# Optimization experiments

Hardware: AMD Instinct MI355X
Metric: run time of the kernel (lower is better)

The kernel has to match this reference:

```python
import jax, jax.numpy as jnp
import numpy as np

B, S, H, E, V, T, OOV = 32, 400, 256, 300, 50000, 20, 50


def setup_inputs() -> dict:
    key = jax.random.key(0)
    ks = jax.random.split(key, 24)
    g = lambda k, sh, scale=0.02: jax.random.normal(k, sh, dtype=jnp.float32) * scale
    return {
        "enc_hidden": jax.random.normal(ks[0], (B, S, 2 * H), dtype=jnp.float32),
        "h0": jax.random.normal(ks[1], (B, H), dtype=jnp.float32),
        "c0": jax.random.normal(ks[2], (B, H), dtype=jnp.float32),
        "embedding": g(ks[3], (V, E), 1.0),
        "W_enc": g(ks[4], (2 * H, H)),
        "W_dec": g(ks[5], (H, H)),
        "w_cov": g(ks[6], (H,)),
        "v_attn": g(ks[7], (H,)),
        "W_ih": g(ks[8], (E, 4 * H)),
        "W_hh": g(ks[9], (H, 4 * H)),
        "b_lstm": jnp.zeros((4 * H,), jnp.float32),
        "W_out1": g(ks[10], (3 * H, H)),
        "b_out1": jnp.zeros((H,), jnp.float32),
        "W_out2": g(ks[11], (H, V)),
        "b_out2": jnp.zeros((V,), jnp.float32),
        "w_h": g(ks[12], (2 * H, 1)),
        "w_s": g(ks[13], (H, 1)),
        "w_x": g(ks[14], (E, 1)),
        "b_x": jnp.zeros((1,), jnp.float32),
        "dec_input": jax.random.randint(ks[15], (B, T), 0, V),
        "enc_input_ext": jax.random.randint(ks[16], (B, S), 0, V + OOV),
        "enc_pad_mask": jnp.ones((B, S), dtype=bool),
        "max_oov_len": OOV,
    }


def reference(enc_hidden, h0, c0, embedding, W_enc, W_dec, w_cov, v_attn,
              W_ih, W_hh, b_lstm, W_out1, b_out1, W_out2, b_out2,
              w_h, w_s, w_x, b_x, dec_input, enc_input_ext, enc_pad_mask,
              max_oov_len):
    b, s, two_h = enc_hidden.shape
    enc_feat = enc_hidden @ W_enc  # [B,S,H], precomputed attention keys
    batch_idx = jnp.arange(b)[:, None]
    NEG = jnp.float32(-1e9)

    def step(carry, x_t):
        h, c, cov = carry
        emb = embedding[x_t]  # [B,E]
        # LSTM cell
        gates = emb @ W_ih + h @ W_hh + b_lstm
        i, f, gg, o = jnp.split(gates, 4, axis=-1)
        c = jax.nn.sigmoid(f) * c + jax.nn.sigmoid(i) * jnp.tanh(gg)
        h = jax.nn.sigmoid(o) * jnp.tanh(c)
        # coverage attention over encoder states
        e = jnp.tanh(enc_feat + (h @ W_dec)[:, None, :] + cov[..., None] * w_cov) @ v_attn  # [B,S]
        e = jnp.where(enc_pad_mask, e, NEG)
        attn = jax.nn.softmax(e, axis=-1)
        context = jnp.einsum('bs,bsd->bd', attn, enc_hidden)  # [B,2H]
        cov = cov + attn
        # vocab distribution
        out = jnp.concatenate([h, context], axis=-1) @ W_out1 + b_out1
        vocab_dist = jax.nn.softmax(out @ W_out2 + b_out2, axis=-1)  # [B,V]
        # pointer-generator gate
        p_gen = jax.nn.sigmoid(context @ w_h + h @ w_s + emb @ w_x + b_x)  # [B,1]
        vocab_dist = p_gen * vocab_dist
        weighted_attn = (1.0 - p_gen) * attn
        # extend vocab and scatter-add copy probabilities
        ext = jnp.concatenate(
            [vocab_dist, jnp.zeros((b, max_oov_len), vocab_dist.dtype)], axis=-1)
        final = ext.at[batch_idx, enc_input_ext].add(weighted_attn)
        return (h, c, cov), (final, attn, cov)

    cov0 = jnp.zeros((b, s), jnp.float32)
    _, (finals, attns, covs) = jax.lax.scan(step, (h0, c0, cov0), dec_input.T)
    # stack with time on the last axis, as in the torch module
    return (jnp.moveaxis(finals, 0, -1),
            jnp.moveaxis(attns, 0, -1),
            jnp.moveaxis(covs, 0, -1))
```

## Files before the change

kernel.cpp:

```cpp
#include <hip/hip_runtime.h>
#include <hip/hip_bf16.h>

#define B_    32
#define S_    400
#define H_    256
#define E_    300
#define V_    50000
#define T_    20
#define VE_   50050
#define TB_   640
#define VPAD_ 50048
#define FIN_  32032000
#define NB_   16
#define SC_   25
#define K5NT  8

typedef __attribute__((ext_vector_type(8))) short bf16x8;
typedef __attribute__((ext_vector_type(4))) float f32x4;

__device__ __forceinline__ float sigmoid_f(float x){ return 1.f/(1.f+__expf(-x)); }
__device__ __forceinline__ float tanh_f(float x){ return 1.f - 2.f/(__expf(2.f*x)+1.f); }

__device__ __forceinline__ float bf2f(unsigned short u){
  union { unsigned int i; float f; } x; x.i = ((unsigned int)u) << 16; return x.f;
}
__device__ __forceinline__ unsigned short f2bf(float f){
  union { __hip_bfloat16 h; unsigned short u; } x; x.h = __float2bfloat16(f); return x.u;
}

__device__ __forceinline__ void st_dev(float* p, float v){
  __hip_atomic_store(p, v, __ATOMIC_RELAXED, __HIP_MEMORY_SCOPE_AGENT);
}
__device__ __forceinline__ float ld_dev(const float* p){
  return __hip_atomic_load(p, __ATOMIC_RELAXED, __HIP_MEMORY_SCOPE_AGENT);
}
__device__ __forceinline__ int ld_cnt(const int* p){
  return __hip_atomic_load(p, __ATOMIC_RELAXED, __HIP_MEMORY_SCOPE_AGENT);
}
__device__ __forceinline__ void add_cnt(int* p){
  __hip_atomic_fetch_add(p, 1, __ATOMIC_RELAXED, __HIP_MEMORY_SCOPE_AGENT);
}


__global__ __launch_bounds__(256) void kT(const float* __restrict__ in,
                                          __hip_bfloat16* __restrict__ out, int R, int C){
  __shared__ float tile[32][33];
  int tx = threadIdx.x & 31, ty = threadIdx.x >> 5;
  int c = blockIdx.x*32 + tx;
  #pragma unroll
  for (int i = 0; i < 4; ++i){
    int r = blockIdx.y*32 + ty + i*8;
    if (r < R && c < C) tile[ty + i*8][tx] = in[(size_t)r*C + c];
  }
  __syncthreads();
  int r2 = blockIdx.y*32 + tx;
  #pragma unroll
  for (int i = 0; i < 4; ++i){
    int c2 = blockIdx.x*32 + ty + i*8;
    if (r2 < R && c2 < C) out[(size_t)c2*R + r2] = __float2bfloat16(tile[tx][ty + i*8]);
  }
}

__global__ __launch_bounds__(256) void kpair2(const float* __restrict__ Whh,
                                              const float* __restrict__ Wdec,
                                              unsigned short* __restrict__ oW,
                                              unsigned short* __restrict__ oD){
  int g = blockIdx.x*256 + threadIdx.x;
  if (g < 262144){
    int k = g >> 10, n = g & 1023;
    oW[(size_t)(k >> 1)*2048 + n*2 + (k & 1)] = f2bf(Whh[g]);
  } else {
    int g2 = g - 262144;
    int k = g2 >> 8, n = g2 & 255;
    oD[(size_t)(k >> 1)*512 + n*2 + (k & 1)] = f2bf(Wdec[g2]);
  }
}

__global__ __launch_bounds__(256) void k1s(const float* __restrict__ emb,
                                           const int* __restrict__ dec,
                                           const float* __restrict__ W_ih,
                                           const float* __restrict__ b_lstm,
                                           float* __restrict__ pre_ih){
  int m = blockIdx.x;
  int r0 = m*2, r1 = m*2 + 1;
  int tid = threadIdx.x;
  __shared__ float e0[304], e1[304];
  int g0 = dec[(r0 & 31)*20 + (r0 >> 5)];
  int g1 = dec[(r1 & 31)*20 + (r1 >> 5)];
  for (int k = tid; k < 300; k += 256){
    e0[k] = emb[(size_t)g0*300 + k];
    e1[k] = emb[(size_t)g1*300 + k];
  }
  __syncthreads();
  float a0[4] = {}, a1[4] = {};
  #pragma unroll 4
  for (int k = 0; k < 300; ++k){
    const float* wr = W_ih + (size_t)k*1024 + tid;
    float w0 = wr[0], w1 = wr[256], w2 = wr[512], w3 = wr[768];
    float x0 = e0[k], x1 = e1[k];
    a0[0] += x0*w0; a0[1] += x0*w1; a0[2] += x0*w2; a0[3] += x0*w3;
    a1[0] += x1*w0; a1[1] += x1*w1; a1[2] += x1*w2; a1[3] += x1*w3;
  }
  #pragma unroll
  for (int j = 0; j < 4; ++j){
    float bl = b_lstm[tid + j*256];
    pre_ih[(size_t)r0*1024 + tid + j*256] = a0[j] + bl;
    pre_ih[(size_t)r1*1024 + tid + j*256] = a1[j] + bl;
  }
}

__global__ __launch_bounds__(256) void k2(const float* __restrict__ EH,
                                          const __hip_bfloat16* __restrict__ Bt,
                                          __hip_bfloat16* __restrict__ Cbf){
  int tid = threadIdx.x;
  int lane = tid & 63, wave = tid >> 6;
  int wm = wave >> 1, wn = wave & 1;
  int n0 = blockIdx.x*128, m0 = blockIdx.y*128;
  __shared__ __align__(16) unsigned short A_s[128][40];
  __shared__ __align__(16) unsigned short B_s[128][40];
  f32x4 acc[4][4];
  #pragma unroll
  for (int i = 0; i < 4; ++i)
    #pragma unroll
    for (int j = 0; j < 4; ++j) acc[i][j] = (f32x4){0.f,0.f,0.f,0.f};
  int cg = tid & 3;
  for (int kc = 0; kc < 16; ++kc){
    __syncthreads();
    #pragma unroll
    for (int rr = 0; rr < 2; ++rr){
      int row = (tid >> 2) + rr*64;
      const float* src = EH + (size_t)(m0+row)*512 + kc*32 + cg*8;
      float4 f0 = *(const float4*)src;
      float4 f1 = *(const float4*)(src + 4);
      unsigned int u0 = ((unsigned int)f2bf(f0.y) << 16) | f2bf(f0.x);
      unsigned int u1 = ((unsigned int)f2bf(f0.w) << 16) | f2bf(f0.z);
      unsigned int u2 = ((unsigned int)f2bf(f1.y) << 16) | f2bf(f1.x);
      unsigned int u3 = ((unsigned int)f2bf(f1.w) << 16) | f2bf(f1.z);
      unsigned int* dst = (unsigned int*)&A_s[row][cg*8];
      dst[0] = u0; dst[1] = u1; dst[2] = u2; dst[3] = u3;
      *(float4*)&B_s[row][cg*8] = *(const float4*)(Bt + (size_t)(n0+row)*512 + kc*32 + cg*8);
    }
    __syncthreads();
    bf16x8 af[4], bfr[4];
    #pragma unroll
    for (int mt = 0; mt < 4; ++mt)
      af[mt] = *(const bf16x8*)&A_s[wm*64 + mt*16 + (lane & 15)][(lane >> 4)*8];
    #pragma unroll
    for (int nt = 0; nt < 4; ++nt)
      bfr[nt] = *(const bf16x8*)&B_s[wn*64 + nt*16 + (lane & 15)][(lane >> 4)*8];
    #pragma unroll
    for (int mt = 0; mt < 4; ++mt)
      #pragma unroll
      for (int nt = 0; nt < 4; ++nt)
        acc[mt][nt] = __builtin_amdgcn_mfma_f32_16x16x32_bf16(af[mt], bfr[nt], acc[mt][nt], 0, 0, 0);
  }
  int lm = lane & 15, lq = lane >> 4;
  #pragma unroll
  for (int mt = 0; mt < 4; ++mt)
    #pragma unroll
    for (int nt = 0; nt < 4; ++nt){
      int vv = n0 + wn*64 + nt*16 + lm;
      #pragma unroll
      for (int rg = 0; rg < 4; ++rg){
        int r = m0 + wm*64 + mt*16 + lq*4 + rg;
        Cbf[(size_t)r*256 + vv] = __float2bfloat16(acc[mt][nt][rg]);
      }
    }
}

__global__ __launch_bounds__(256) void krec(
    const float* __restrict__ h0, const float* __restrict__ c0,
    const unsigned short* __restrict__ Whh2,
    const unsigned short* __restrict__ Wd2,
    const float* __restrict__ w_cov, const float* __restrict__ v_attn,
    const float* __restrict__ pre_ih, const __hip_bfloat16* __restrict__ enc_feat,
    const float* __restrict__ enc_hidden,
    float* __restrict__ H_all, float* __restrict__ exps_g,
    float* __restrict__ Zatt, float* __restrict__ ctxp,
    float* __restrict__ hdecp, int* bar)
{
  const int bx = blockIdx.x;
  const int b = (bx & 7) + 8*((bx >> 3) & 3);
  const int jj = bx >> 5;
  const int tid = threadIdx.x;
  const int lane = tid & 63, wave = tid >> 6;
  const int s0 = jj*SC_;

  __shared__ __align__(16) unsigned short eh_s[SC_][512];
  __shared__ __align__(16) unsigned short ef_s[SC_][256];
  __shared__ float h_pad[272];
  __shared__ float hdec_sh[256], vat[256], wcv[256];
  __shared__ float h_loc[16];
  __shared__ float covf[32], ehist[2][32];
  __shared__ float invZ_sh;

  for (int e = tid; e < SC_*128; e += 256){
    int row = e >> 7, c4 = e & 127;
    float4 f = *(const float4*)(enc_hidden + ((size_t)(b*400 + s0 + row))*512 + c4*4);
    unsigned int lo = ((unsigned int)f2bf(f.y) << 16) | f2bf(f.x);
    unsigned int hi = ((unsigned int)f2bf(f.w) << 16) | f2bf(f.z);
    *(unsigned int*)&eh_s[row][c4*4]     = lo;
    *(unsigned int*)&eh_s[row][c4*4 + 2] = hi;
  }
  for (int e = tid; e < SC_*32; e += 256){
    int row = e >> 5, c8 = e & 31;
    *(float4*)&ef_s[row][c8*8] =
      *(const float4*)(enc_feat + ((size_t)(b*400 + s0 + row))*256 + c8*8);
  }
  vat[tid] = v_attn[tid];
  wcv[tid] = w_cov[tid];
  h_pad[tid + 4*(tid >> 6)] = h0[b*256 + tid];
  if (tid < 32) covf[tid] = 0.f;

  const int kq = lane & 3, cl = (lane >> 2) & 3, gt = lane >> 4;
  const int ci = wave*4 + cl;
  const int gcol = gt*256 + jj*16 + ci;
  ushort2 wreg[32];
  #pragma unroll
  for (int pp = 0; pp < 32; ++pp)
    wreg[pp] = *(const ushort2*)(Whh2 + ((size_t)(kq*32 + pp))*2048 + gcol*2);
  ushort2 wdreg[8];
  #pragma unroll
  for (int p = 0; p < 8; ++p)
    wdreg[p] = *(const ushort2*)(Wd2 + ((size_t)(jj*8 + p))*512 + tid*2);
  float c_reg = c0[b*256 + jj*16 + ci];

  __syncthreads();

  int* cnt_h = bar + b*16;
  int* cnt_z = cnt_h + 4;

  {
    float acc = (kq == 0) ? pre_ih[(size_t)b*1024 + gcol] : 0.f;
    const float* hb = &h_pad[kq*68];
    #pragma unroll
    for (int pp = 0; pp < 32; ++pp){
      float2 h2 = *(const float2*)&hb[pp*2];
      acc += h2.x*bf2f(wreg[pp].x) + h2.y*bf2f(wreg[pp].y);
    }
    acc += __shfl_xor(acc, 1);
    acc += __shfl_xor(acc, 2);
    int base = lane & 12;
    float gi = __shfl(acc, base);
    float gf = __shfl(acc, base + 16);
    float gG = __shfl(acc, base + 32);
    float go = __shfl(acc, base + 48);
    float cn = sigmoid_f(gf)*c_reg + sigmoid_f(gi)*tanh_f(gG);
    c_reg = cn;
    float hv = sigmoid_f(go)*tanh_f(cn);
    if ((lane & 51) == 0){
      st_dev(&H_all[(size_t)b*256 + jj*16 + ci], hv);
      h_loc[ci] = hv;
    }
  }
  __syncthreads();
  {
    float pd = 0.f;
    #pragma unroll
    for (int p = 0; p < 8; ++p)
      pd += h_loc[p*2]*bf2f(wdreg[p].x) + h_loc[p*2 + 1]*bf2f(wdreg[p].y);
    st_dev(&hdecp[((size_t)b*16 + jj)*256 + tid], pd);
  }
  __syncthreads();
  if (tid == 0) add_cnt(cnt_h);

  #pragma unroll 1
  for (int t = 0; t < T_; ++t){
    const int r = t*32 + b;
    float pihn = (kq == 0 && t < T_-1) ? pre_ih[(size_t)(r+32)*1024 + gcol] : 0.f;
    if (tid == 0){
      while (ld_cnt(cnt_h) < NB_*(t + 1)) __builtin_amdgcn_s_sleep(1);
    }
    __syncthreads();
    {
      float hfull = ld_dev(&H_all[(size_t)r*256 + tid]);
      float hd = 0.f;
      #pragma unroll
      for (int j2 = 0; j2 < 16; ++j2)
        hd += ld_dev(&hdecp[((size_t)r*16 + j2)*256 + tid]);
      h_pad[tid + 4*(tid >> 6)] = hfull;
      hdec_sh[tid] = hd;
    }
    __syncthreads();
    if (t < T_-1){
      float acc = pihn;
      const float* hb = &h_pad[kq*68];
      #pragma unroll
      for (int pp = 0; pp < 32; ++pp){
        float2 h2 = *(const float2*)&hb[pp*2];
        acc += h2.x*bf2f(wreg[pp].x) + h2.y*bf2f(wreg[pp].y);
      }
      acc += __shfl_xor(acc, 1);
      acc += __shfl_xor(acc, 2);
      int base = lane & 12;
      float gi = __shfl(acc, base);
      float gf = __shfl(acc, base + 16);
      float gG = __shfl(acc, base + 32);
      float go = __shfl(acc, base + 48);
      float cn = sigmoid_f(gf)*c_reg + sigmoid_f(gi)*tanh_f(gG);
      c_reg = cn;
      float hv = sigmoid_f(go)*tanh_f(cn);
      if ((lane & 51) == 0){
        st_dev(&H_all[(size_t)(r+32)*256 + jj*16 + ci], hv);
        h_loc[ci] = hv;
      }
    }
    __syncthreads();
    if (t < T_-1){
      float pd = 0.f;
      #pragma unroll
      for (int p = 0; p < 8; ++p)
        pd += h_loc[p*2]*bf2f(wdreg[p].x) + h_loc[p*2 + 1]*bf2f(wdreg[p].y);
      st_dev(&hdecp[((size_t)(r+32)*16 + jj)*256 + tid], pd);
    }
    __syncthreads();
    if (tid == 0){
      if (t < T_-1) add_cnt(cnt_h);
      if (t > 0){
        while (ld_cnt(cnt_z) < NB_*t) __builtin_amdgcn_s_sleep(1);
        invZ_sh = 1.f/ld_dev(&Zatt[r - 32]);
      }
    }
    __syncthreads();
    float* ecur = ehist[t & 1];
    const float* eprev = ehist[(t ^ 1) & 1];
    float invz = invZ_sh;
    for (int sl = wave; sl < SC_; sl += 4){
      float cw = covf[sl];
      if (t > 0) cw += eprev[sl]*invz;
      float part = 0.f;
      #pragma unroll
      for (int q = 0; q < 4; ++q){
        int k = lane + q*64;
        float x = bf2f(ef_s[sl][k]) + hdec_sh[k] + cw*wcv[k];
        part += vat[k]*tanh_f(x);
      }
      #pragma unroll
      for (int off = 32; off > 0; off >>= 1) part += __shfl_xor(part, off);
      if (lane == 0){
        covf[sl] = cw;
        float ev = __expf(part);
        ecur[sl] = ev;
        exps_g[(size_t)r*400 + s0 + sl] = ev;
      }
    }
    __syncthreads();
    if (tid == 0){
      float z = 0.f;
      #pragma unroll
      for (int q = 0; q < SC_; ++q) z += ecur[q];
      atomicAdd(&Zatt[r], z);
      asm volatile("s_waitcnt vmcnt(0)" ::: "memory");
      add_cnt(cnt_z);
    }
    #pragma unroll
    for (int hh = 0; hh < 2; ++hh){
      int d = tid + hh*256;
      float a2 = 0.f;
      #pragma unroll
      for (int sl = 0; sl < SC_; ++sl) a2 += ecur[sl]*bf2f(eh_s[sl][d]);
      ctxp[((size_t)r*16 + jj)*512 + d] = a2;
    }
  }
}

__global__ __launch_bounds__(256) void k3a(const float* __restrict__ Zatt,
                                           const float* __restrict__ ctxp,
                                           const float* __restrict__ H_all,
                                           const float* __restrict__ w_h,
                                           const float* __restrict__ w_s,
                                           const float* __restrict__ emb,
                                           const int* __restrict__ dec,
                                           const float* __restrict__ w_x,
                                           const float* __restrict__ b_x,
                                           float* __restrict__ CAT,
                                           float* __restrict__ pgen){
  int r = blockIdx.x, tid = threadIdx.x;
  __shared__ float red[256];
  float invz = 1.f/Zatt[r];
  float hv = H_all[(size_t)r*256 + tid];
  CAT[(size_t)r*768 + tid] = hv;
  float a0 = 0.f, a1 = 0.f;
  const float* p = ctxp + (size_t)r*16*512;
  #pragma unroll
  for (int jj = 0; jj < 16; ++jj){
    a0 += p[jj*512 + tid];
    a1 += p[jj*512 + 256 + tid];
  }
  float cv0 = a0*invz;
  float cv1 = a1*invz;
  CAT[(size_t)r*768 + 256 + tid] = cv0;
  CAT[(size_t)r*768 + 512 + tid] = cv1;
  int gid = dec[(r & 31)*20 + (r >> 5)];
  float px = 0.f;
  for (int k = tid; k < 300; k += 256) px += emb[(size_t)gid*300 + k]*w_x[k];
  float pg = hv*w_s[tid] + cv0*w_h[tid] + cv1*w_h[tid + 256];
  red[tid] = pg + px; __syncthreads();
  for (int st = 128; st > 0; st >>= 1){
    if (tid < st) red[tid] += red[tid + st];
    __syncthreads();
  }
  if (tid == 0) pgen[r] = sigmoid_f(red[0] + b_x[0]);
}

__global__ __launch_bounds__(256) void k3b(const float* __restrict__ exps_g,
                                           const float* __restrict__ Zatt,
                                           float* __restrict__ attns,
                                           float* __restrict__ covs){
  __shared__ float tA[256*20];
  __shared__ float tC[256*20];
  int tid = threadIdx.x;
  int g0 = blockIdx.x*256;
  int g = g0 + tid;
  int b = g / 400, s = g % 400;
  float cum = 0.f;
  for (int t = 0; t < T_; ++t){
    int r = t*32 + b;
    float a = exps_g[(size_t)r*400 + s] / Zatt[r];
    cum += a;
    tA[tid*20 + t] = a;
    tC[tid*20 + t] = cum;
  }
  __syncthreads();
  size_t base = (size_t)g0*20;
  for (int e = tid; e < 5120; e += 256){
    attns[base + e] = tA[e];
    covs[base + e]  = tC[e];
  }
}

__global__ __launch_bounds__(256) void k4s(const float* __restrict__ CAT,
                                           const float* __restrict__ W1,
                                           const float* __restrict__ b1,
                                           __hip_bfloat16* __restrict__ OUTb){
  int m = blockIdx.x, tid = threadIdx.x;
  int r0 = m*2, r1 = r0 + 1;
  __shared__ float c0s[768], c1s[768];
  for (int k = tid; k < 768; k += 256){
    c0s[k] = CAT[(size_t)r0*768 + k];
    c1s[k] = CAT[(size_t)r1*768 + k];
  }
  __syncthreads();
  float a0 = 0.f, a1 = 0.f;
  #pragma unroll 4
  for (int k = 0; k < 768; ++k){
    float w = W1[(size_t)k*256 + tid];
    a0 += c0s[k]*w;
    a1 += c1s[k]*w;
  }
  float bb = b1[tid];
  OUTb[(size_t)r0*256 + tid] = __float2bfloat16(a0 + bb);
  OUTb[(size_t)r1*256 + tid] = __float2bfloat16(a1 + bb);
}

__global__ __launch_bounds__(256) void k5(const __hip_bfloat16* __restrict__ OUTb,
                                          const __hip_bfloat16* __restrict__ W2t,
                                          const float* __restrict__ b_out2,
                                          __hip_bfloat16* __restrict__ temp,
                                          float* __restrict__ Zsum){
  int tid = threadIdx.x;
  int lane = tid & 63, wave = tid >> 6;
  int wm = wave >> 1, wn = wave & 1;
  int m0 = blockIdx.x*128;
  int ng = blockIdx.y;
  __shared__ __align__(16) unsigned short A_s[128][264];
  __shared__ __align__(16) unsigned short B_s[128][264];
  for (int e = tid; e < 4096; e += 256){
    int row = e >> 5, c8 = e & 31;
    *(float4*)&A_s[row][c8*8] = *(const float4*)(OUTb + (size_t)(m0 + row)*256 + c8*8);
  }
  int lm = lane & 15, lq = lane >> 4;
  #pragma unroll 1
  for (int ti = 0; ti < K5NT; ++ti){
    int n0 = (ng*K5NT + ti)*128;
    if (n0 >= VPAD_) break;
    __syncthreads();
    for (int e = tid; e < 4096; e += 256){
      int row = e >> 5, c8 = e & 31;
      int v = n0 + row;
      float4 bv = make_float4(0.f, 0.f, 0.f, 0.f);
      if (v < V_) bv = *(const float4*)(W2t + (size_t)v*256 + c8*8);
      *(float4*)&B_s[row][c8*8] = bv;
    }
    __syncthreads();
    f32x4 acc[4][4];
    #pragma unroll
    for (int i = 0; i < 4; ++i)
      #pragma unroll
      for (int j = 0; j < 4; ++j) acc[i][j] = (f32x4){0.f,0.f,0.f,0.f};
    #pragma unroll
    for (int ks = 0; ks < 8; ++ks){
      bf16x8 af[4], bfr[4];
      #pragma unroll
      for (int mt = 0; mt < 4; ++mt)
        af[mt] = *(const bf16x8*)&A_s[wm*64 + mt*16 + lm][lq*8 + ks*32];
      #pragma unroll
      for (int nt = 0; nt < 4; ++nt)
        bfr[nt] = *(const bf16x8*)&B_s[wn*64 + nt*16 + lm][lq*8 + ks*32];
      #pragma unroll
      for (int mt = 0; mt < 4; ++mt)
        #pragma unroll
        for (int nt = 0; nt < 4; ++nt)
          acc[mt][nt] = __builtin_amdgcn_mfma_f32_16x16x32_bf16(af[mt], bfr[nt], acc[mt][nt], 0, 0, 0);
    }
    float rowsum[4][4];
    #pragma unroll
    for (int mt = 0; mt < 4; ++mt)
      #pragma unroll
      for (int rg = 0; rg < 4; ++rg) rowsum[mt][rg] = 0.f;
    #pragma unroll
    for (int mt = 0; mt < 4; ++mt)
      #pragma unroll
      for (int nt = 0; nt < 4; ++nt){
        int vv = n0 + wn*64 + nt*16 + lm;
        float b2 = (vv < V_) ? b_out2[vv] : 0.f;
        #pragma unroll
        for (int rg = 0; rg < 4; ++rg){
          int r = m0 + wm*64 + mt*16 + lq*4 + rg;
          float e = __expf(acc[mt][nt][rg] + b2);
          temp[(size_t)r*VPAD_ + vv] = __float2bfloat16(e);
          if (vv >= V_) e = 0.f;
          rowsum[mt][rg] += e;
        }
      }
    #pragma unroll
    for (int mt = 0; mt < 4; ++mt)
      #pragma unroll
      for (int rg = 0; rg < 4; ++rg){
        float s = rowsum[mt][rg];
        s += __shfl_xor(s, 1); s += __shfl_xor(s, 2);
        s += __shfl_xor(s, 4); s += __shfl_xor(s, 8);
        if (lm == 0){
          int r = m0 + wm*64 + mt*16 + lq*4 + rg;
          atomicAdd(&Zsum[r], s);
        }
      }
  }
}

__global__ __launch_bounds__(256) void k6(const __hip_bfloat16* __restrict__ temp,
                                          const float* __restrict__ pgen,
                                          const float* __restrict__ Zsum,
                                          float* __restrict__ finals){
  int b = blockIdx.y, cb = blockIdx.x, tid = threadIdx.x;
  int v0 = cb*512;
  __shared__ float tile[20][513];
  __shared__ float ssc[20];
  if (tid < 20){ int r = tid*32 + b; ssc[tid] = pgen[r]/Zsum[r]; }
  __syncthreads();
  for (int e = tid; e < 1280; e += 256){
    int tt = e >> 6, c8 = e & 63;
    int v = v0 + c8*8;
    float sc = ssc[tt];
    const __hip_bfloat16* src = temp + (size_t)(tt*32 + b)*VPAD_ + v;
    if (v + 7 < V_){
      float4 raw = *(const float4*)src;
      const unsigned short* u = (const unsigned short*)&raw;
      #pragma unroll
      for (int j = 0; j < 8; ++j) tile[tt][c8*8 + j] = bf2f(u[j])*sc;
    } else {
      #pragma unroll
      for (int j = 0; j < 8; ++j)
        tile[tt][c8*8 + j] = (v + j < V_) ? __bfloat162float(src[j])*sc : 0.f;
    }
  }
  __syncthreads();
  int wlim = (VE_ - v0)*20; if (wlim > 10240) wlim = 10240;
  float* dst = finals + (size_t)b*1001000 + (size_t)v0*20;
  for (int e = tid; e < wlim; e += 256){
    dst[e] = tile[e % 20][e / 20];
  }
}

__global__ __launch_bounds__(320) void k7(const float* __restrict__ exps_g,
                                          const float* __restrict__ Zatt,
                                          const float* __restrict__ pgen,
                                          const int* __restrict__ ext,
                                          float* __restrict__ finals){
  int tid = threadIdx.x;
  int g = blockIdx.x*16 + tid/20;
  int t = tid % 20;
  int b = g / 400, s = g % 400;
  int r = t*32 + b;
  int idx = ext[g];
  float w = (1.f - pgen[r])*exps_g[(size_t)r*400 + s]/Zatt[r];
  atomicAdd(finals + (size_t)b*1001000 + (size_t)idx*20 + t, w);
}

extern "C" void kernel_launch(void* const* d_in, const int* in_sizes, int n_in,
                              void* d_out, int out_size, void* d_ws, size_t ws_size,
                              hipStream_t stream){
  const float* enc_hidden = (const float*)d_in[0];
  const float* h0         = (const float*)d_in[1];
  const float* c0         = (const float*)d_in[2];
  const float* embedding  = (const float*)d_in[3];
  const float* W_enc      = (const float*)d_in[4];
  const float* W_dec      = (const float*)d_in[5];
  const float* w_cov      = (const float*)d_in[6];
  const float* v_attn     = (const float*)d_in[7];
  const float* W_ih       = (const float*)d_in[8];
  const float* W_hh       = (const float*)d_in[9];
  const float* b_lstm     = (const float*)d_in[10];
  const float* W_out1     = (const float*)d_in[11];
  const float* b_out1     = (const float*)d_in[12];
  const float* W_out2     = (const float*)d_in[13];
  const float* b_out2     = (const float*)d_in[14];
  const float* w_h        = (const float*)d_in[15];
  const float* w_s        = (const float*)d_in[16];
  const float* w_x        = (const float*)d_in[17];
  const float* b_x        = (const float*)d_in[18];
  const int*   dec_input  = (const int*)d_in[19];
  const int*   enc_ext    = (const int*)d_in[20];

  float* out    = (float*)d_out;
  float* finals = out;
  float* attns  = out + FIN_;
  float* covs   = out + FIN_ + 256000;

  char* w = (char*)d_ws;
  auto alloc = [&](size_t n){ char* p = w; w += (n + 255) & ~(size_t)255; return p; };
  int*   bar      = (int*)  alloc(32*64);
  float* Zsum     = (float*)alloc((size_t)TB_*4);
  float* Zatt     = (float*)alloc((size_t)TB_*4);
  float* pre_ih   = (float*)alloc((size_t)TB_*1024*4);
  unsigned short* Whh2 = (unsigned short*)alloc((size_t)256*1024*2);
  unsigned short* Wd2  = (unsigned short*)alloc((size_t)256*256*2);
  __hip_bfloat16* WencT    = (__hip_bfloat16*)alloc((size_t)256*512*2);
  __hip_bfloat16* W2t      = (__hip_bfloat16*)alloc((size_t)V_*256*2);
  __hip_bfloat16* enc_feat = (__hip_bfloat16*)alloc((size_t)12800*256*2);
  float* H_all    = (float*)alloc((size_t)TB_*256*4);
  float* exps_g   = (float*)alloc((size_t)TB_*400*4);
  float* CAT      = (float*)alloc((size_t)TB_*768*4);
  float* pgen     = (float*)alloc((size_t)TB_*4);
  __hip_bfloat16* OUTb = (__hip_bfloat16*)alloc((size_t)TB_*256*2);
  __hip_bfloat16* temp = (__hip_bfloat16*)alloc((size_t)TB_*VPAD_*2);
  float* ctxp     = (float*)temp;
  float* hdecp    = (float*)((char*)temp + (size_t)TB_*16*512*4);

  hipMemsetAsync(bar, 0, 32*64, stream);
  hipMemsetAsync(Zsum, 0, (size_t)TB_*4, stream);
  hipMemsetAsync(Zatt, 0, (size_t)TB_*4, stream);

  kT <<<dim3(8, 16), 256, 0, stream>>>(W_enc, WencT, 512, 256);
  kT <<<dim3(1563, 8), 256, 0, stream>>>(W_out2, W2t, 256, V_);
  kpair2<<<1280, 256, 0, stream>>>(W_hh, W_dec, Whh2, Wd2);
  k1s<<<320, 256, 0, stream>>>(embedding, dec_input, W_ih, b_lstm, pre_ih);
  k2 <<<dim3(2, 100), 256, 0, stream>>>(enc_hidden, WencT, enc_feat);
  krec<<<512, 256, 0, stream>>>(h0, c0, Whh2, Wd2, w_cov, v_attn, pre_ih,
                                enc_feat, enc_hidden,
                                H_all, exps_g, Zatt, ctxp, hdecp, bar);
  k3a<<<640, 256, 0, stream>>>(Zatt, ctxp, H_all, w_h, w_s,
                               embedding, dec_input, w_x, b_x, CAT, pgen);
  k3b<<<50, 256, 0, stream>>>(exps_g, Zatt, attns, covs);
  k4s<<<320, 256, 0, stream>>>(CAT, W_out1, b_out1, OUTb);
  k5 <<<dim3(5, 49), 256, 0, stream>>>(OUTb, W2t, b_out2, temp, Zsum);
  k6 <<<dim3(98, 32), 256, 0, stream>>>(temp, pgen, Zsum, finals);
  k7 <<<800, 320, 0, stream>>>(exps_g, Zatt, pgen, enc_ext, finals);
}
```

Measured before the change: 793.4 us.

## Merge prep kernels, fuse copy scatter into vocab write, replace Zsum atomics

Folds the transposes, weight packing, input-gate precompute and workspace zeroing into one launch, which removes three memsets and three launches. It also merges k3a and k3b into a single kernel. The pointer scatter-add now runs in shared memory inside the final vocab-write kernel, so the separate global-atomic pass over the 128 MB output is gone. k5 now writes per-block partial softmax sums instead of issuing atomics, and k67 reduces those partials. The cost is more branching in the merged kernels and a 98-element serial reduction per row.

Result: faster. 770.9 us (-2.8%).

```diff
diff --git a/kernel.cpp b/kernel.cpp
--- a/kernel.cpp
+++ b/kernel.cpp
@@ -15,6 +15,12 @@
 #define SC_   25
 #define K5NT  8
 
+#define NP_T2   12504
+#define NP_TE   128
+#define NP_PAIR 1280
+#define NP_K1   320
+#define NP_ALL  (NP_T2 + NP_TE + NP_PAIR + NP_K1 + 1)
+
 typedef __attribute__((ext_vector_type(8))) short bf16x8;
 typedef __attribute__((ext_vector_type(4))) float f32x4;
 
@@ -41,71 +47,82 @@
   __hip_atomic_fetch_add(p, 1, __ATOMIC_RELAXED, __HIP_MEMORY_SCOPE_AGENT);
 }
 
-
-__global__ __launch_bounds__(256) void kT(const float* __restrict__ in,
-                                          __hip_bfloat16* __restrict__ out, int R, int C){
+__global__ __launch_bounds__(256) void kprep(
+    const float* __restrict__ W_out2, __hip_bfloat16* __restrict__ W2t,
+    const float* __restrict__ W_enc,  __hip_bfloat16* __restrict__ WencT,
+    const float* __restrict__ Whh, const float* __restrict__ Wdec,
+    unsigned short* __restrict__ oW, unsigned short* __restrict__ oD,
+    const float* __restrict__ emb, const int* __restrict__ dec,
+    const float* __restrict__ W_ih, const float* __restrict__ b_lstm,
+    float* __restrict__ pre_ih,
+    int* __restrict__ bar, float* __restrict__ Zatt)
+{
+  int blk = blockIdx.x;
+  int tid = threadIdx.x;
   __shared__ float tile[32][33];
-  int tx = threadIdx.x & 31, ty = threadIdx.x >> 5;
-  int c = blockIdx.x*32 + tx;
-  #pragma unroll
-  for (int i = 0; i < 4; ++i){
-    int r = blockIdx.y*32 + ty + i*8;
-    if (r < R && c < C) tile[ty + i*8][tx] = in[(size_t)r*C + c];
-  }
-  __syncthreads();
-  int r2 = blockIdx.y*32 + tx;
-  #pragma unroll
-  for (int i = 0; i < 4; ++i){
-    int c2 = blockIdx.x*32 + ty + i*8;
-    if (r2 < R && c2 < C) out[(size_t)c2*R + r2] = __float2bfloat16(tile[tx][ty + i*8]);
-  }
-}
-
-__global__ __launch_bounds__(256) void kpair2(const float* __restrict__ Whh,
-                                              const float* __restrict__ Wdec,
-                                              unsigned short* __restrict__ oW,
-                                              unsigned short* __restrict__ oD){
-  int g = blockIdx.x*256 + threadIdx.x;
-  if (g < 262144){
-    int k = g >> 10, n = g & 1023;
-    oW[(size_t)(k >> 1)*2048 + n*2 + (k & 1)] = f2bf(Whh[g]);
+  __shared__ float e0[304], e1[304];
+  if (blk < NP_T2 + NP_TE){
+    const float* in; __hip_bfloat16* out; int R, C, bx, by;
+    if (blk < NP_T2){
+      in = W_out2; out = W2t; R = 256; C = 50000;
+      bx = blk % 1563; by = blk / 1563;
+    } else {
+      int q = blk - NP_T2;
+      in = W_enc; out = WencT; R = 512; C = 256;
+      bx = q & 7; by = q >> 3;
+    }
+    int tx = tid & 31, ty = tid >> 5;
+    int c = bx*32 + tx;
+    #pragma unroll
+    for (int i = 0; i < 4; ++i){
+      int r = by*32 + ty + i*8;
+      if (r < R && c < C) tile[ty + i*8][tx] = in[(size_t)r*C + c];
+    }
+    __syncthreads();
+    int r2 = by*32 + tx;
+    #pragma unroll
+    for (int i = 0; i < 4; ++i){
+      int c2 = bx*32 + ty + i*8;
+      if (r2 < R && c2 < C) out[(size_t)c2*R + r2] = __float2bfloat16(tile[tx][ty + i*8]);
+    }
+  } else if (blk < NP_T2 + NP_TE + NP_PAIR){
+    int g = (blk - NP_T2 - NP_TE)*256 + tid;
+    if (g < 262144){
+      int k = g >> 10, n = g & 1023;
+      oW[(size_t)(k >> 1)*2048 + n*2 + (k & 1)] = f2bf(Whh[g]);
+    } else {
+      int g2 = g - 262144;
+      int k = g2 >> 8, n = g2 & 255;
+      oD[(size_t)(k >> 1)*512 + n*2 + (k & 1)] = f2bf(Wdec[g2]);
+    }
+  } else if (blk < NP_T2 + NP_TE + NP_PAIR + NP_K1){
+    int m = blk - NP_T2 - NP_TE - NP_PAIR;
+    int r0 = m*2, r1 = m*2 + 1;
+    int g0 = dec[(r0 & 31)*20 + (r0 >> 5)];
+    int g1 = dec[(r1 & 31)*20 + (r1 >> 5)];
+    for (int k = tid; k < 300; k += 256){
+      e0[k] = emb[(size_t)g0*300 + k];
+      e1[k] = emb[(size_t)g1*300 + k];
+    }
+    __syncthreads();
+    float a0[4] = {}, a1[4] = {};
+    #pragma unroll 4
+    for (int k = 0; k < 300; ++k){
+      const float* wr = W_ih + (size_t)k*1024 + tid;
+      float w0 = wr[0], w1 = wr[256], w2 = wr[512], w3 = wr[768];
+      float x0 = e0[k], x1 = e1[k];
+      a0[0] += x0*w0; a0[1] += x0*w1; a0[2] += x0*w2; a0[3] += x0*w3;
+      a1[0] += x1*w0; a1[1] += x1*w1; a1[2] += x1*w2; a1[3] += x1*w3;
+    }
+    #pragma unroll
+    for (int j = 0; j < 4; ++j){
+      float bl = b_lstm[tid + j*256];
+      pre_ih[(size_t)r0*1024 + tid + j*256] = a0[j] + bl;
+      pre_ih[(size_t)r1*1024 + tid + j*256] = a1[j] + bl;
+    }
   } else {
-    int g2 = g - 262144;
-    int k = g2 >> 8, n = g2 & 255;
-    oD[(size_t)(k >> 1)*512 + n*2 + (k & 1)] = f2bf(Wdec[g2]);
-  }
-}
-
-__global__ __launch_bounds__(256) void k1s(const float* __restrict__ emb,
-                                           const int* __restrict__ dec,
-                                           const float* __restrict__ W_ih,
-                                           const float* __restrict__ b_lstm,
-                                           float* __restrict__ pre_ih){
-  int m = blockIdx.x;
-  int r0 = m*2, r1 = m*2 + 1;
-  int tid = threadIdx.x;
-  __shared__ float e0[304], e1[304];
-  int g0 = dec[(r0 & 31)*20 + (r0 >> 5)];
-  int g1 = dec[(r1 & 31)*20 + (r1 >> 5)];
-  for (int k = tid; k < 300; k += 256){
-    e0[k] = emb[(size_t)g0*300 + k];
-    e1[k] = emb[(size_t)g1*300 + k];
-  }
-  __syncthreads();
-  float a0[4] = {}, a1[4] = {};
-  #pragma unroll 4
-  for (int k = 0; k < 300; ++k){
-    const float* wr = W_ih + (size_t)k*1024 + tid;
-    float w0 = wr[0], w1 = wr[256], w2 = wr[512], w3 = wr[768];
-    float x0 = e0[k], x1 = e1[k];
-    a0[0] += x0*w0; a0[1] += x0*w1; a0[2] += x0*w2; a0[3] += x0*w3;
-    a1[0] += x1*w0; a1[1] += x1*w1; a1[2] += x1*w2; a1[3] += x1*w3;
-  }
-  #pragma unroll
-  for (int j = 0; j < 4; ++j){
-    float bl = b_lstm[tid + j*256];
-    pre_ih[(size_t)r0*1024 + tid + j*256] = a0[j] + bl;
-    pre_ih[(size_t)r1*1024 + tid + j*256] = a1[j] + bl;
+    for (int e = tid; e < 512; e += 256) bar[e] = 0;
+    for (int e = tid; e < 640; e += 256) Zatt[e] = 0.f;
   }
 }
 
@@ -364,68 +381,68 @@
   }
 }
 
-__global__ __launch_bounds__(256) void k3a(const float* __restrict__ Zatt,
-                                           const float* __restrict__ ctxp,
-                                           const float* __restrict__ H_all,
-                                           const float* __restrict__ w_h,
-                                           const float* __restrict__ w_s,
-                                           const float* __restrict__ emb,
-                                           const int* __restrict__ dec,
-                                           const float* __restrict__ w_x,
-                                           const float* __restrict__ b_x,
-                                           float* __restrict__ CAT,
-                                           float* __restrict__ pgen){
-  int r = blockIdx.x, tid = threadIdx.x;
+__global__ __launch_bounds__(256) void k3ab(const float* __restrict__ Zatt,
+                                            const float* __restrict__ ctxp,
+                                            const float* __restrict__ H_all,
+                                            const float* __restrict__ w_h,
+                                            const float* __restrict__ w_s,
+                                            const float* __restrict__ emb,
+                                            const int* __restrict__ dec,
+                                            const float* __restrict__ w_x,
+                                            const float* __restrict__ b_x,
+                                            const float* __restrict__ exps_g,
+                                            float* __restrict__ CAT,
+                                            float* __restrict__ pgen,
+                                            float* __restrict__ attns,
+                                            float* __restrict__ covs){
+  int blk = blockIdx.x, tid = threadIdx.x;
   __shared__ float red[256];
-  float invz = 1.f/Zatt[r];
-  float hv = H_all[(size_t)r*256 + tid];
-  CAT[(size_t)r*768 + tid] = hv;
-  float a0 = 0.f, a1 = 0.f;
-  const float* p = ctxp + (size_t)r*16*512;
-  #pragma unroll
-  for (int jj = 0; jj < 16; ++jj){
-    a0 += p[jj*512 + tid];
-    a1 += p[jj*512 + 256 + tid];
-  }
-  float cv0 = a0*invz;
-  float cv1 = a1*invz;
-  CAT[(size_t)r*768 + 256 + tid] = cv0;
-  CAT[(size_t)r*768 + 512 + tid] = cv1;
-  int gid = dec[(r & 31)*20 + (r >> 5)];
-  float px = 0.f;
-  for (int k = tid; k < 300; k += 256) px += emb[(size_t)gid*300 + k]*w_x[k];
-  float pg = hv*w_s[tid] + cv0*w_h[tid] + cv1*w_h[tid + 256];
-  red[tid] = pg + px; __syncthreads();
-  for (int st = 128; st > 0; st >>= 1){
-    if (tid < st) red[tid] += red[tid + st];
-    __syncthreads();
-  }
-  if (tid == 0) pgen[r] = sigmoid_f(red[0] + b_x[0]);
-}
-
-__global__ __launch_bounds__(256) void k3b(const float* __restrict__ exps_g,
-                                           const float* __restrict__ Zatt,
-                                           float* __restrict__ attns,
-                                           float* __restrict__ covs){
   __shared__ float tA[256*20];
   __shared__ float tC[256*20];
-  int tid = threadIdx.x;
-  int g0 = blockIdx.x*256;
-  int g = g0 + tid;
-  int b = g / 400, s = g % 400;
-  float cum = 0.f;
-  for (int t = 0; t < T_; ++t){
-    int r = t*32 + b;
-    float a = exps_g[(size_t)r*400 + s] / Zatt[r];
-    cum += a;
-    tA[tid*20 + t] = a;
-    tC[tid*20 + t] = cum;
-  }
-  __syncthreads();
-  size_t base = (size_t)g0*20;
-  for (int e = tid; e < 5120; e += 256){
-    attns[base + e] = tA[e];
-    covs[base + e]  = tC[e];
+  if (blk < 640){
+    int r = blk;
+    float invz = 1.f/Zatt[r];
+    float hv = H_all[(size_t)r*256 + tid];
+    CAT[(size_t)r*768 + tid] = hv;
+    float a0 = 0.f, a1 = 0.f;
+    const float* p = ctxp + (size_t)r*16*512;
+    #pragma unroll
+    for (int jj = 0; jj < 16; ++jj){
+      a0 += p[jj*512 + tid];
+      a1 += p[jj*512 + 256 + tid];
+    }
+    float cv0 = a0*invz;
+    float cv1 = a1*invz;
+    CAT[(size_t)r*768 + 256 + tid] = cv0;
+    CAT[(size_t)r*768 + 512 + tid] = cv1;
+    int gid = dec[(r & 31)*20 + (r >> 5)];
+    float px = 0.f;
+    for (int k = tid; k < 300; k += 256) px += emb[(size_t)gid*300 + k]*w_x[k];
+    float pg = hv*w_s[tid] + cv0*w_h[tid] + cv1*w_h[tid + 256];
+    red[tid] = pg + px; __syncthreads();
+    for (int st = 128; st > 0; st >>= 1){
+      if (tid < st) red[tid] += red[tid + st];
+      __syncthreads();
+    }
+    if (tid == 0) pgen[r] = sigmoid_f(red[0] + b_x[0]);
+  } else {
+    int g0 = (blk - 640)*256;
+    int g = g0 + tid;
+    int b = g / 400, s = g % 400;
+    float cum = 0.f;
+    for (int t = 0; t < T_; ++t){
+      int r = t*32 + b;
+      float a = exps_g[(size_t)r*400 + s] / Zatt[r];
+      cum += a;
+      tA[tid*20 + t] = a;
+      tC[tid*20 + t] = cum;
+    }
+    __syncthreads();
+    size_t base = (size_t)g0*20;
+    for (int e = tid; e < 5120; e += 256){
+      attns[base + e] = tA[e];
+      covs[base + e]  = tC[e];
+    }
   }
 }
 
@@ -457,7 +474,7 @@
                                           const __hip_bfloat16* __restrict__ W2t,
                                           const float* __restrict__ b_out2,
                                           __hip_bfloat16* __restrict__ temp,
-                                          float* __restrict__ Zsum){
+                                          float* __restrict__ Zsump){
   int tid = threadIdx.x;
   int lane = tid & 63, wave = tid >> 6;
   int wm = wave >> 1, wn = wave & 1;
@@ -470,6 +487,11 @@
     *(float4*)&A_s[row][c8*8] = *(const float4*)(OUTb + (size_t)(m0 + row)*256 + c8*8);
   }
   int lm = lane & 15, lq = lane >> 4;
+  float zacc[4][4];
+  #pragma unroll
+  for (int mt = 0; mt < 4; ++mt)
+    #pragma unroll
+    for (int rg = 0; rg < 4; ++rg) zacc[mt][rg] = 0.f;
   #pragma unroll 1
   for (int ti = 0; ti < K5NT; ++ti){
     int n0 = (ng*K5NT + ti)*128;
@@ -530,23 +552,42 @@
         float s = rowsum[mt][rg];
         s += __shfl_xor(s, 1); s += __shfl_xor(s, 2);
         s += __shfl_xor(s, 4); s += __shfl_xor(s, 8);
-        if (lm == 0){
-          int r = m0 + wm*64 + mt*16 + lq*4 + rg;
-          atomicAdd(&Zsum[r], s);
-        }
-      }
-  }
-}
-
-__global__ __launch_bounds__(256) void k6(const __hip_bfloat16* __restrict__ temp,
-                                          const float* __restrict__ pgen,
-                                          const float* __restrict__ Zsum,
-                                          float* __restrict__ finals){
+        zacc[mt][rg] += s;
+      }
+  }
+  if (lm == 0){
+    #pragma unroll
+    for (int mt = 0; mt < 4; ++mt)
+      #pragma unroll
+      for (int rg = 0; rg < 4; ++rg){
+        int r = m0 + wm*64 + mt*16 + lq*4 + rg;
+        Zsump[(size_t)r*98 + ng*2 + wn] = zacc[mt][rg];
+      }
+  }
+}
+
+__global__ __launch_bounds__(256) void k67(const __hip_bfloat16* __restrict__ temp,
+                                           const float* __restrict__ pgen,
+                                           const float* __restrict__ Zsump,
+                                           const float* __restrict__ exps_g,
+                                           const float* __restrict__ Zatt,
+                                           const int* __restrict__ ext,
+                                           float* __restrict__ finals){
   int b = blockIdx.y, cb = blockIdx.x, tid = threadIdx.x;
   int v0 = cb*512;
   __shared__ float tile[20][513];
-  __shared__ float ssc[20];
-  if (tid < 20){ int r = tid*32 + b; ssc[tid] = pgen[r]/Zsum[r]; }
+  __shared__ float ssc[20], wts[20];
+  __shared__ int ex_s[400];
+  if (tid < 20){
+    int r = tid*32 + b;
+    float zs = 0.f;
+    const float* zp = Zsump + (size_t)r*98;
+    for (int q = 0; q < 98; ++q) zs += zp[q];
+    float pg = pgen[r];
+    ssc[tid] = pg/zs;
+    wts[tid] = (1.f - pg)/Zatt[r];
+  }
+  for (int e = tid; e < 400; e += 256) ex_s[e] = ext[b*400 + e];
   __syncthreads();
   for (int e = tid; e < 1280; e += 256){
     int tt = e >> 6, c8 = e & 63;
@@ -565,26 +606,23 @@
     }
   }
   __syncthreads();
+  for (int s = tid; s < 400; s += 256){
+    int idx = ex_s[s];
+    if (idx >= v0 && idx < v0 + 512){
+      #pragma unroll
+      for (int t = 0; t < T_; ++t){
+        int r = t*32 + b;
+        float w = wts[t]*exps_g[(size_t)r*400 + s];
+        atomicAdd(&tile[t][idx - v0], w);
+      }
+    }
+  }
+  __syncthreads();
   int wlim = (VE_ - v0)*20; if (wlim > 10240) wlim = 10240;
   float* dst = finals + (size_t)b*1001000 + (size_t)v0*20;
   for (int e = tid; e < wlim; e += 256){
     dst[e] = tile[e % 20][e / 20];
   }
-}
-
-__global__ __launch_bounds__(320) void k7(const float* __restrict__ exps_g,
-                                          const float* __restrict__ Zatt,
-                                          const float* __restrict__ pgen,
-                                          const int* __restrict__ ext,
-                                          float* __restrict__ finals){
-  int tid = threadIdx.x;
-  int g = blockIdx.x*16 + tid/20;
-  int t = tid % 20;
-  int b = g / 400, s = g % 400;
-  int r = t*32 + b;
-  int idx = ext[g];
-  float w = (1.f - pgen[r])*exps_g[(size_t)r*400 + s]/Zatt[r];
-  atomicAdd(finals + (size_t)b*1001000 + (size_t)idx*20 + t, w);
 }
 
 extern "C" void kernel_launch(void* const* d_in, const int* in_sizes, int n_in,
@@ -620,8 +658,8 @@
   char* w = (char*)d_ws;
   auto alloc = [&](size_t n){ char* p = w; w += (n + 255) & ~(size_t)255; return p; };
   int*   bar      = (int*)  alloc(32*64);
-  float* Zsum     = (float*)alloc((size_t)TB_*4);
   float* Zatt     = (float*)alloc((size_t)TB_*4);
+  float* Zsump    = (float*)alloc((size_t)TB_*98*4);
   float* pre_ih   = (float*)alloc((size_t)TB_*1024*4);
   unsigned short* Whh2 = (unsigned short*)alloc((size_t)256*1024*2);
   unsigned short* Wd2  = (unsigned short*)alloc((size_t)256*256*2);
@@ -637,23 +675,19 @@
   float* ctxp     = (float*)temp;
   float* hdecp    = (float*)((char*)temp + (size_t)TB_*16*512*4);
 
-  hipMemsetAsync(bar, 0, 32*64, stream);
-  hipMemsetAsync(Zsum, 0, (size_t)TB_*4, stream);
-  hipMemsetAsync(Zatt, 0, (size_t)TB_*4, stream);
-
-  kT <<<dim3(8, 16), 256, 0, stream>>>(W_enc, WencT, 512, 256);
-  kT <<<dim3(1563, 8), 256, 0, stream>>>(W_out2, W2t, 256, V_);
-  kpair2<<<1280, 256, 0, stream>>>(W_hh, W_dec, Whh2, Wd2);
-  k1s<<<320, 256, 0, stream>>>(embedding, dec_input, W_ih, b_lstm, pre_ih);
+  kprep<<<NP_ALL, 256, 0, stream>>>(W_out2, W2t, W_enc, WencT,
+                                    W_hh, W_dec, Whh2, Wd2,
+                                    embedding, dec_input, W_ih, b_lstm, pre_ih,
+                                    bar, Zatt);
   k2 <<<dim3(2, 100), 256, 0, stream>>>(enc_hidden, WencT, enc_feat);
   krec<<<512, 256, 0, stream>>>(h0, c0, Whh2, Wd2, w_cov, v_attn, pre_ih,
                                 enc_feat, enc_hidden,
                                 H_all, exps_g, Zatt, ctxp, hdecp, bar);
-  k3a<<<640, 256, 0, stream>>>(Zatt, ctxp, H_all, w_h, w_s,
-                               embedding, dec_input, w_x, b_x, CAT, pgen);
-  k3b<<<50, 256, 0, stream>>>(exps_g, Zatt, attns, covs);
+  k3ab<<<690, 256, 0, stream>>>(Zatt, ctxp, H_all, w_h, w_s,
+                                embedding, dec_input, w_x, b_x, exps_g,
+                                CAT, pgen, attns, covs);
   k4s<<<320, 256, 0, stream>>>(CAT, W_out1, b_out1, OUTb);
-  k5 <<<dim3(5, 49), 256, 0, stream>>>(OUTb, W2t, b_out2, temp, Zsum);
-  k6 <<<dim3(98, 32), 256, 0, stream>>>(temp, pgen, Zsum, finals);
-  k7 <<<800, 320, 0, stream>>>(exps_g, Zatt, pgen, enc_ext, finals);
-}
+  k5 <<<dim3(5, 49), 256, 0, stream>>>(OUTb, W2t, b_out2, temp, Zsump);
+  k67<<<dim3(98, 32), 256, 0, stream>>>(temp, pgen, Zsump, exps_g, Zatt,
+                                        enc_ext, finals);
+}
```
